# Optimization experiments

Measured on AMD Instinct MI355X. Metric: run time of the kernel, lower is better.

## Reference

```python
import jax, jax.numpy as jnp
import numpy as np

DIM, HEADS, MLP_HID = 1024, 16, 4096
B, N = 2, 2048
EPS = 1e-5

def setup_inputs() -> dict:
    key = jax.random.key(0)
    ks = jax.random.split(key, 8)
    s = lambda fan_in: 1.0 / np.sqrt(fan_in)
    return {
        "x": jax.random.normal(ks[0], (B, N, DIM), jnp.float32),
        "ln1_w": jnp.ones((DIM,), jnp.float32),
        "ln1_b": jnp.zeros((DIM,), jnp.float32),
        # weights stored [in, out] (transpose of torch Linear.weight)
        "qkv_w": jax.random.normal(ks[1], (DIM, 3 * DIM), jnp.float32) * s(DIM),
        "proj_w": jax.random.normal(ks[2], (DIM, DIM), jnp.float32) * s(DIM),
        "proj_b": jnp.zeros((DIM,), jnp.float32),
        "ln2_w": jnp.ones((DIM,), jnp.float32),
        "ln2_b": jnp.zeros((DIM,), jnp.float32),
        "fc1_w": jax.random.normal(ks[3], (DIM, MLP_HID), jnp.float32) * s(DIM),
        "fc1_b": jnp.zeros((MLP_HID,), jnp.float32),
        "fc2_w": jax.random.normal(ks[4], (MLP_HID, DIM), jnp.float32) * s(MLP_HID),
        "fc2_b": jnp.zeros((DIM,), jnp.float32),
    }

def _layernorm(x, w, b):
    mu = jnp.mean(x, axis=-1, keepdims=True)
    var = jnp.mean(jnp.square(x - mu), axis=-1, keepdims=True)
    return (x - mu) * jax.lax.rsqrt(var + EPS) * w + b

def reference(x, ln1_w, ln1_b, qkv_w, proj_w, proj_b, ln2_w, ln2_b, fc1_w, fc1_b, fc2_w, fc2_b):
    Bn, Nn, C = x.shape
    H, D = HEADS, C // HEADS
    scale = D ** -0.5

    # --- attention sub-block (pre-norm, residual) ---
    h = _layernorm(x, ln1_w, ln1_b)
    qkv = (h @ qkv_w).reshape(Bn, Nn, 3, H, D)
    q, k, v = jnp.moveaxis(qkv, 2, 0)  # each [B, N, H, D]
    attn = jnp.einsum('bnhd,bmhd->bhnm', q, k) * scale
    attn = jax.nn.softmax(attn, axis=-1)
    o = jnp.einsum('bhnm,bmhd->bnhd', attn, v).reshape(Bn, Nn, C)
    x = x + (o @ proj_w + proj_b)

    # --- MLP sub-block (pre-norm, residual) ---
    h = _layernorm(x, ln2_w, ln2_b)
    h = jax.nn.gelu(h @ fc1_w + fc1_b, approximate=False)
    x = x + (h @ fc2_w + fc2_b)
    return x
```

## Files before the change

### kernel.cpp

```cpp
#include <hip/hip_runtime.h>
#include <hip/hip_bf16.h>

typedef __attribute__((ext_vector_type(4))) float  f32x4;
typedef __attribute__((ext_vector_type(8))) short  short8;
typedef __attribute__((ext_vector_type(8))) unsigned short ushort8;
typedef __attribute__((ext_vector_type(4))) unsigned short u16x4;
typedef unsigned short u16;

__device__ __forceinline__ u16 f2bf(float f) {
    unsigned int u = __builtin_bit_cast(unsigned int, f);
    return (u16)((u + 0x7fffu + ((u >> 16) & 1u)) >> 16);
}

__device__ __forceinline__ unsigned cvtpk(float lo, float hi) {
    unsigned r;
    asm("v_cvt_pk_bf16_f32 %0, %1, %2" : "=v"(r) : "v"(lo), "v"(hi));
    return r;
}

__device__ __forceinline__ f32x4 mfma16(short8 a, short8 b, f32x4 c) {
    return __builtin_amdgcn_mfma_f32_16x16x32_bf16(a, b, c, 0, 0, 0);
}

__device__ __forceinline__ float fexp2(float x) {
    float r;
    asm("v_exp_f32 %0, %1" : "=v"(r) : "v"(x));
    return r;
}

__device__ __forceinline__ float fgelu(float v) {
    const float t = v * v;
    const float u = v * (-2.302118f - 0.102944f * t);
    return v / (1.0f + fexp2(u));
}

__device__ __forceinline__ void gload_lds16(const u16* g, u16* l) {
    __builtin_amdgcn_global_load_lds(
        (__attribute__((address_space(1))) void*)(uintptr_t)(g),
        (__attribute__((address_space(3))) void*)(unsigned)(uintptr_t)(l),
        16, 0, 0);
}

__device__ __forceinline__ void tcast_body(const float* __restrict__ W,
                                           u16* __restrict__ Wt,
                                           int K, int N, int bx, int by) {
    __shared__ float tile[32][33];
    const int tx = threadIdx.x & 31, ty = threadIdx.x >> 5;
    const int c0 = bx * 32;
    const int r0 = by * 32;
#pragma unroll
    for (int i = 0; i < 32; i += 8)
        tile[ty + i][tx] = W[(size_t)(r0 + ty + i) * N + c0 + tx];
    __syncthreads();
#pragma unroll
    for (int i = 0; i < 32; i += 8)
        Wt[(size_t)(c0 + ty + i) * K + r0 + tx] = f2bf(tile[tx][ty + i]);
}

__device__ __forceinline__ void ln_body(const float* __restrict__ x,
                                        const float* __restrict__ w,
                                        const float* __restrict__ b,
                                        u16* __restrict__ out, int row) {
    const int tid = threadIdx.x;
    const float4 v = ((const float4*)(x + (size_t)row * 1024))[tid];
    float s1 = v.x + v.y + v.z + v.w;
    float s2 = v.x * v.x + v.y * v.y + v.z * v.z + v.w * v.w;
#pragma unroll
    for (int m = 1; m < 64; m <<= 1) { s1 += __shfl_xor(s1, m); s2 += __shfl_xor(s2, m); }
    __shared__ float red1[4], red2[4];
    const int wave = tid >> 6, lane = tid & 63;
    if (lane == 0) { red1[wave] = s1; red2[wave] = s2; }
    __syncthreads();
    s1 = red1[0] + red1[1] + red1[2] + red1[3];
    s2 = red2[0] + red2[1] + red2[2] + red2[3];
    const float mean = s1 * (1.0f / 1024.0f);
    const float var  = s2 * (1.0f / 1024.0f) - mean * mean;
    const float rstd = rsqrtf(var + 1e-5f);
    const float4 wv = ((const float4*)w)[tid];
    const float4 bv = ((const float4*)b)[tid];
    u16x4 o;
    o[0] = f2bf((v.x - mean) * rstd * wv.x + bv.x);
    o[1] = f2bf((v.y - mean) * rstd * wv.y + bv.y);
    o[2] = f2bf((v.z - mean) * rstd * wv.z + bv.z);
    o[3] = f2bf((v.w - mean) * rstd * wv.w + bv.w);
    *(u16x4*)(out + (size_t)row * 1024 + tid * 4) = o;
}

__global__ __launch_bounds__(256) void prep1_kernel(const float* __restrict__ x,
                                                    const float* __restrict__ ln1w,
                                                    const float* __restrict__ ln1b,
                                                    u16* __restrict__ h1,
                                                    const float* __restrict__ qkvw,
                                                    u16* __restrict__ wt_qkv) {
    int id = blockIdx.x;
    if (id < 4096) { ln_body(x, ln1w, ln1b, h1, id); return; }
    id -= 4096;
    tcast_body(qkvw, wt_qkv, 1024, 3072, id % 96, id / 96);
}

__global__ __launch_bounds__(256) void ln_kernel(const float* __restrict__ x,
                                                 const float* __restrict__ w,
                                                 const float* __restrict__ b,
                                                 u16* __restrict__ out) {
    ln_body(x, w, b, out, blockIdx.x);
}

__device__ __forceinline__ void tcast_body512(const float* __restrict__ W,
                                              u16* __restrict__ Wt,
                                              int K, int N, int bx, int by,
                                              float (*tile)[33]) {
    const int tx = threadIdx.x & 31, ty = threadIdx.x >> 5;
    const int c0 = bx * 32;
    const int r0 = by * 32;
#pragma unroll
    for (int i = 0; i < 32; i += 16)
        tile[ty + i][tx] = W[(size_t)(r0 + ty + i) * N + c0 + tx];
    __syncthreads();
#pragma unroll
    for (int i = 0; i < 32; i += 16)
        Wt[(size_t)(c0 + ty + i) * K + r0 + tx] = f2bf(tile[tx][ty + i]);
}

__global__ __launch_bounds__(512, 2) void qkvfused_kernel(const u16* __restrict__ A,
                                                          const u16* __restrict__ Bt,
                                                          u16* __restrict__ Cout,
                                                          u16* __restrict__ vt,
                                                          const float* __restrict__ projw,
                                                          u16* __restrict__ wt_proj,
                                                          const float* __restrict__ fc1w,
                                                          u16* __restrict__ wt_fc1,
                                                          const float* __restrict__ fc2w,
                                                          u16* __restrict__ wt_fc2) {
    __shared__ __align__(16) u16 Ag[3][256 * 32];
    __shared__ __align__(16) u16 Bg[3][128 * 32];
    __shared__ float tile[32][33];
    constexpr int K = 1024, N = 3072;

    if (blockIdx.x >= 384) {
        int id = blockIdx.x - 384;
        if (id < 1024) { tcast_body512(projw, wt_proj, 1024, 1024, id % 32, id / 32, tile); return; }
        id -= 1024;
        if (id < 4096) { tcast_body512(fc1w, wt_fc1, 1024, 4096, id % 128, id / 128, tile); return; }
        id -= 4096;
        tcast_body512(fc2w, wt_fc2, 4096, 1024, id % 32, id / 32, tile);
        return;
    }

    const int tid = threadIdx.x;
    const int wave = tid >> 6, lane = tid & 63;
    const int wr = wave >> 2, wc = wave & 3;
    const int fq = lane >> 4, fr = lane & 15;

    int bid = blockIdx.x;
    bid = (bid & 7) * 48 + (bid >> 3);
    const size_t bm = (size_t)(bid / 24) * 256, bn = (size_t)(bid % 24) * 128;

    const int ko = (fq ^ ((fr >> 1) & 3)) * 8;

    const int srow = tid >> 2;
    const int scol = ((tid & 3) ^ ((tid >> 3) & 3)) * 8;
    const u16* Asrc = A  + (bm + srow) * (size_t)K + scol;
    const u16* Bsrc = Bt + (bn + srow) * (size_t)K + scol;
    const int sdst = wave * 512;

    f32x4 acc[8][2] = {};

    auto STAGE_G = [&](int slot, int kc) {
        gload_lds16(Asrc + kc,                      &Ag[slot][sdst]);
        gload_lds16(Asrc + (size_t)128 * K + kc,    &Ag[slot][sdst + 4096]);
        gload_lds16(Bsrc + kc,                      &Bg[slot][sdst]);
    };

    const int NG = K >> 5;
    STAGE_G(0, 0); STAGE_G(1, 32);
    asm volatile("s_waitcnt vmcnt(3)" ::: "memory");
    __builtin_amdgcn_s_barrier();

    int slot = 0;
    for (int g = 0; g < NG; g++) {
        short8 bfr[2], af[4];
#pragma unroll
        for (int nt = 0; nt < 2; nt++)
            bfr[nt] = *(const short8*)&Bg[slot][(wc * 32 + nt * 16 + fr) * 32 + ko];
#pragma unroll
        for (int m2 = 0; m2 < 4; m2++)
            af[m2] = *(const short8*)&Ag[slot][(wr * 128 + m2 * 16 + fr) * 32 + ko];
        if (g + 2 < NG) {
            const int s2 = slot >= 1 ? slot - 1 : slot + 2;
            STAGE_G(s2, (g + 2) * 32);
        }
        __builtin_amdgcn_s_barrier();
        __builtin_amdgcn_s_setprio(1);
#pragma unroll
        for (int m2 = 0; m2 < 4; m2++)
#pragma unroll
            for (int nt = 0; nt < 2; nt++)
                acc[m2][nt] = mfma16(af[m2], bfr[nt], acc[m2][nt]);
        __builtin_amdgcn_s_setprio(0);
        __builtin_amdgcn_s_barrier();
#pragma unroll
        for (int m2 = 0; m2 < 4; m2++)
            af[m2] = *(const short8*)&Ag[slot][(wr * 128 + (m2 + 4) * 16 + fr) * 32 + ko];
        __builtin_amdgcn_s_barrier();
        __builtin_amdgcn_s_setprio(1);
#pragma unroll
        for (int m2 = 0; m2 < 4; m2++)
#pragma unroll
            for (int nt = 0; nt < 2; nt++)
                acc[m2 + 4][nt] = mfma16(af[m2], bfr[nt], acc[m2 + 4][nt]);
        __builtin_amdgcn_s_setprio(0);
        if (g < NG - 2) { asm volatile("s_waitcnt vmcnt(3)" ::: "memory"); }
        else            { asm volatile("s_waitcnt vmcnt(0)" ::: "memory"); }
        __builtin_amdgcn_s_barrier();
        slot = slot == 2 ? 0 : slot + 1;
    }
    if (bn >= 2048) {
#pragma unroll
        for (int mt = 0; mt < 8; mt++) {
#pragma unroll
            for (int nt = 0; nt < 2; nt++) {
                const size_t col = (bn - 2048) + wc * 32 + nt * 16 + fr;
                const size_t row = bm + wr * 128 + mt * 16 + fq * 4;
                const size_t n = row & 2047, bb = row >> 11;
                u16x4 pw;
#pragma unroll
                for (int j = 0; j < 4; j++) pw[j] = f2bf(acc[mt][nt][j]);
                *(u16x4*)&vt[(bb * 1024 + col) * 2048 + n] = pw;
            }
        }
    } else {
#pragma unroll
        for (int mt = 0; mt < 8; mt++) {
#pragma unroll
            for (int nt = 0; nt < 2; nt++) {
                const size_t col = bn + wc * 32 + nt * 16 + fr;
#pragma unroll
                for (int j = 0; j < 4; j++) {
                    const size_t row = bm + wr * 128 + mt * 16 + fq * 4 + j;
                    Cout[row * N + col] = f2bf(acc[mt][nt][j]);
                }
            }
        }
    }
}

template <int HAS_BIAS, int HAS_RES, int DO_GELU, int OUT_BF16>
__global__ __launch_bounds__(512, 2) void gemm8_kernel(const u16* __restrict__ A,
                                                       const u16* __restrict__ Bt,
                                                       const float* __restrict__ bias,
                                                       const float* __restrict__ res,
                                                       void* __restrict__ Cout,
                                                       int M, int N, int K) {
    __shared__ __align__(16) u16 Ag[3][256 * 32];
    __shared__ __align__(16) u16 Bg[3][128 * 32];
    const int tid = threadIdx.x;
    const int wave = tid >> 6, lane = tid & 63;
    const int wr = wave >> 2, wc = wave & 3;
    const int fq = lane >> 4, fr = lane & 15;

    const int gx = gridDim.x;
    const int nwg = gx * gridDim.y;
    int bid = blockIdx.y * gx + blockIdx.x;
    bid = (bid & 7) * (nwg >> 3) + (bid >> 3);
    const size_t bm = (size_t)(bid / gx) * 256, bn = (size_t)(bid % gx) * 128;

    const int ko = (fq ^ ((fr >> 1) & 3)) * 8;

    const int srow = tid >> 2;
    const int scol = ((tid & 3) ^ ((tid >> 3) & 3)) * 8;
    const u16* Asrc = A  + (bm + srow) * (size_t)K + scol;
    const u16* Bsrc = Bt + (bn + srow) * (size_t)K + scol;
    const int sdst = wave * 512;

    f32x4 acc[8][2] = {};

    auto STAGE_G = [&](int slot, int kc) {
        gload_lds16(Asrc + kc,                      &Ag[slot][sdst]);
        gload_lds16(Asrc + (size_t)128 * K + kc,    &Ag[slot][sdst + 4096]);
        gload_lds16(Bsrc + kc,                      &Bg[slot][sdst]);
    };

    const int NG = K >> 5;
    STAGE_G(0, 0); STAGE_G(1, 32);
    asm volatile("s_waitcnt vmcnt(3)" ::: "memory");
    __builtin_amdgcn_s_barrier();

    int slot = 0;
    for (int g = 0; g < NG; g++) {
        short8 bfr[2], af[4];
#pragma unroll
        for (int nt = 0; nt < 2; nt++)
            bfr[nt] = *(const short8*)&Bg[slot][(wc * 32 + nt * 16 + fr) * 32 + ko];
#pragma unroll
        for (int m2 = 0; m2 < 4; m2++)
            af[m2] = *(const short8*)&Ag[slot][(wr * 128 + m2 * 16 + fr) * 32 + ko];
        if (g + 2 < NG) {
            const int s2 = slot >= 1 ? slot - 1 : slot + 2;
            STAGE_G(s2, (g + 2) * 32);
        }
        __builtin_amdgcn_s_barrier();
        __builtin_amdgcn_s_setprio(1);
#pragma unroll
        for (int m2 = 0; m2 < 4; m2++)
#pragma unroll
            for (int nt = 0; nt < 2; nt++)
                acc[m2][nt] = mfma16(af[m2], bfr[nt], acc[m2][nt]);
        __builtin_amdgcn_s_setprio(0);
        __builtin_amdgcn_s_barrier();
#pragma unroll
        for (int m2 = 0; m2 < 4; m2++)
            af[m2] = *(const short8*)&Ag[slot][(wr * 128 + (m2 + 4) * 16 + fr) * 32 + ko];
        __builtin_amdgcn_s_barrier();
        __builtin_amdgcn_s_setprio(1);
#pragma unroll
        for (int m2 = 0; m2 < 4; m2++)
#pragma unroll
            for (int nt = 0; nt < 2; nt++)
                acc[m2 + 4][nt] = mfma16(af[m2], bfr[nt], acc[m2 + 4][nt]);
        __builtin_amdgcn_s_setprio(0);
        if (g < NG - 2) { asm volatile("s_waitcnt vmcnt(3)" ::: "memory"); }
        else            { asm volatile("s_waitcnt vmcnt(0)" ::: "memory"); }
        __builtin_amdgcn_s_barrier();
        slot = slot == 2 ? 0 : slot + 1;
    }
#pragma unroll
    for (int mt = 0; mt < 8; mt++) {
#pragma unroll
        for (int nt = 0; nt < 2; nt++) {
            const size_t col = bn + wc * 32 + nt * 16 + fr;
            const float bb = HAS_BIAS ? bias[col] : 0.0f;
#pragma unroll
            for (int j = 0; j < 4; j++) {
                const size_t row = bm + wr * 128 + mt * 16 + fq * 4 + j;
                float v = acc[mt][nt][j] + bb;
                if (DO_GELU) v = fgelu(v);
                if (HAS_RES) v += res[row * N + col];
                if (OUT_BF16) ((u16*)Cout)[row * N + col] = f2bf(v);
                else          ((float*)Cout)[row * N + col] = v;
            }
        }
    }
}

template <int HAS_BIAS, int HAS_RES, int DO_GELU, int OUT_BF16>
__global__ __launch_bounds__(256) void gemm64_kernel(const u16* __restrict__ A,
                                                     const u16* __restrict__ Bt,
                                                     const float* __restrict__ bias,
                                                     const float* __restrict__ res,
                                                     void* __restrict__ Cout,
                                                     int M, int N, int K) {
    __shared__ __align__(16) u16 As[2][64 * 64];
    __shared__ __align__(16) u16 Bs[2][128 * 64];
    const int tid = threadIdx.x;
    const int wave = tid >> 6, lane = tid & 63;
    const int wc = wave;
    const int fq = lane >> 4, fr = lane & 15;

    const int gx = gridDim.x;
    const int nwg = gx * gridDim.y;
    int bid = blockIdx.y * gx + blockIdx.x;
    bid = (bid & 7) * (nwg >> 3) + (bid >> 3);
    const size_t bm = (size_t)(bid / gx) * 64, bn = (size_t)(bid % gx) * 128;

    const int lr = lane >> 3, seg = lane & 7;
    const int seg2 = seg ^ lr;

    const u16* Ab = A  + bm * (size_t)K + seg2 * 8;
    const u16* Bb = Bt + bn * (size_t)K + seg2 * 8;

    const int rx = fr & 7;
    const int ko0 = ((0 + fq) ^ rx) * 8;
    const int ko1 = ((4 + fq) ^ rx) * 8;

    f32x4 acc[4][2] = {};

    auto STAGE = [&](int buf, int k0) {
#pragma unroll
        for (int s = 0; s < 2; s++)
            gload_lds16(Ab + (size_t)(s * 32 + wave * 8 + lr) * K + k0,
                        &As[buf][s * 2048 + wave * 512]);
#pragma unroll
        for (int s = 0; s < 4; s++)
            gload_lds16(Bb + (size_t)(s * 32 + wave * 8 + lr) * K + k0,
                        &Bs[buf][s * 2048 + wave * 512]);
    };

    STAGE(0, 0);
    __syncthreads();
    int cur = 0;

    for (int k0 = 0; k0 < K; k0 += 64) {
        if (k0 + 64 < K) STAGE(cur ^ 1, k0 + 64);
#pragma unroll
        for (int ks = 0; ks < 2; ks++) {
            const int ko = ks ? ko1 : ko0;
            short8 af[4], bf[2];
#pragma unroll
            for (int t = 0; t < 4; t++)
                af[t] = *(const short8*)&As[cur][(t * 16 + fr) * 64 + ko];
#pragma unroll
            for (int nt = 0; nt < 2; nt++)
                bf[nt] = *(const short8*)&Bs[cur][(wc * 32 + nt * 16 + fr) * 64 + ko];
#pragma unroll
            for (int mt = 0; mt < 4; mt++)
#pragma unroll
                for (int nt = 0; nt < 2; nt++)
                    acc[mt][nt] = mfma16(af[mt], bf[nt], acc[mt][nt]);
        }
        __syncthreads();
        cur ^= 1;
    }
#pragma unroll
    for (int mt = 0; mt < 4; mt++) {
#pragma unroll
        for (int nt = 0; nt < 2; nt++) {
            const size_t col = bn + wc * 32 + nt * 16 + fr;
            const float bb = HAS_BIAS ? bias[col] : 0.0f;
#pragma unroll
            for (int j = 0; j < 4; j++) {
                const size_t row = bm + mt * 16 + fq * 4 + j;
                float v = acc[mt][nt][j] + bb;
                if (DO_GELU) v = fgelu(v);
                if (HAS_RES) v += res[row * N + col];
                if (OUT_BF16) ((u16*)Cout)[row * N + col] = f2bf(v);
                else          ((float*)Cout)[row * N + col] = v;
            }
        }
    }
}

__global__ __launch_bounds__(512) void attn_kernel(const u16* __restrict__ qkv,
                                                   const u16* __restrict__ vt,
                                                   u16* __restrict__ O) {
    const int bh = blockIdx.x;
    const int b = bh >> 4, h = bh & 15;
    const int qb = blockIdx.y;
    const int tid = threadIdx.x, wave = tid >> 6, lane = tid & 63;
    const int fq = lane >> 4, fr = lane & 15;
    __shared__ __align__(16) u16 Ks[2][64 * 64];
    __shared__ __align__(16) u16 Vs[2][64 * 64];
    __shared__ __align__(16) u16 Pl[8][16 * 64];

    const size_t base = (size_t)b * 2048 * 3072;
    const int q0 = qb * 128 + wave * 16;

    short8 qf[2];
#pragma unroll
    for (int ks = 0; ks < 2; ks++)
        qf[ks] = *(const short8*)(qkv + base + (size_t)(q0 + fr) * 3072 + h * 64 + ks * 32 + fq * 8);

    const int srow = tid >> 3, schunk = tid & 7;
    const int spos = (schunk ^ (srow & 7)) * 8;
    const u16* kdma = qkv + base + 1024 + (size_t)h * 64 + (size_t)srow * 3072 + spos;
    const u16* vdma = vt + ((size_t)b * 1024 + h * 64 + srow) * 2048 + spos;
    const int sdst = wave * 512;

    const int rx = fr & 7;
    const int ko0 = ((0 + fq) ^ rx) * 8;
    const int ko1 = ((4 + fq) ^ rx) * 8;

    f32x4 accO[4] = {};
    float lq = 0.0f;

    const float c = 0.125f * 1.44269504f;

    auto STAGE = [&](int buf, int kt) {
        gload_lds16(kdma + (size_t)kt * 64 * 3072, &Ks[buf][sdst]);
        gload_lds16(vdma + kt * 64,                &Vs[buf][sdst]);
    };

    STAGE(0, 0);
    __syncthreads();
    int cur = 0;

    for (int kt = 0; kt < 32; kt++) {
        if (kt < 31) STAGE(cur ^ 1, kt + 1);
        f32x4 s[4];
#pragma unroll
        for (int nt = 0; nt < 4; nt++) {
            f32x4 a = {};
            short8 kf0 = *(const short8*)&Ks[cur][(nt * 16 + fr) * 64 + ko0];
            short8 kf1 = *(const short8*)&Ks[cur][(nt * 16 + fr) * 64 + ko1];
            a = mfma16(kf0, qf[0], a);
            a = mfma16(kf1, qf[1], a);
            s[nt] = a;
        }
#pragma unroll
        for (int nt = 0; nt < 4; nt++)
#pragma unroll
            for (int j = 0; j < 4; j++) {
                const float pij = fexp2(s[nt][j] * c);
                s[nt][j] = pij;
                lq += pij;
            }
#pragma unroll
        for (int nt = 0; nt < 4; nt++) {
            uint2 pw;
            pw.x = cvtpk(s[nt][0], s[nt][1]);
            pw.y = cvtpk(s[nt][2], s[nt][3]);
            const int chunk = nt * 2 + (fq >> 1);
            *(uint2*)&Pl[wave][fr * 64 + (chunk ^ rx) * 8 + (fq & 1) * 4] = pw;
        }
#pragma unroll
        for (int ks = 0; ks < 2; ks++) {
            const int ko = ks ? ko1 : ko0;
            short8 pf = *(const short8*)&Pl[wave][fr * 64 + ko];
#pragma unroll
            for (int dt = 0; dt < 4; dt++) {
                short8 vf = *(const short8*)&Vs[cur][(dt * 16 + fr) * 64 + ko];
                accO[dt] = mfma16(pf, vf, accO[dt]);
            }
        }
        __syncthreads();
        cur ^= 1;
    }
    lq += __shfl_xor(lq, 16);
    lq += __shfl_xor(lq, 32);
    float rq[4];
#pragma unroll
    for (int j = 0; j < 4; j++) rq[j] = 1.0f / __shfl(lq, fq * 4 + j);
#pragma unroll
    for (int dt = 0; dt < 4; dt++)
#pragma unroll
        for (int j = 0; j < 4; j++) {
            const float v = accO[dt][j] * rq[j];
            O[(size_t)(b * 2048 + q0 + fq * 4 + j) * 1024 + h * 64 + dt * 16 + fr] = f2bf(v);
        }
}

extern "C" void kernel_launch(void* const* d_in, const int* in_sizes, int n_in,
                              void* d_out, int out_size, void* d_ws, size_t ws_size,
                              hipStream_t stream) {
    (void)in_sizes; (void)n_in; (void)out_size; (void)ws_size;
    const float* x     = (const float*)d_in[0];
    const float* ln1w  = (const float*)d_in[1];
    const float* ln1b  = (const float*)d_in[2];
    const float* qkvw  = (const float*)d_in[3];
    const float* projw = (const float*)d_in[4];
    const float* projb = (const float*)d_in[5];
    const float* ln2w  = (const float*)d_in[6];
    const float* ln2b  = (const float*)d_in[7];
    const float* fc1w  = (const float*)d_in[8];
    const float* fc1b  = (const float*)d_in[9];
    const float* fc2w  = (const float*)d_in[10];
    const float* fc2b  = (const float*)d_in[11];

    char* p = (char*)d_ws;
    auto alloc = [&](size_t bytes) { void* r = p; p += (bytes + 255) & ~(size_t)255; return r; };
    u16* wt_qkv  = (u16*)alloc(3072ull * 1024 * 2);
    u16* wt_proj = (u16*)alloc(1024ull * 1024 * 2);
    u16* wt_fc1  = (u16*)alloc(4096ull * 1024 * 2);
    u16* wt_fc2  = (u16*)alloc(1024ull * 4096 * 2);
    u16* h1      = (u16*)alloc(4096ull * 1024 * 2);
    u16* qkv     = (u16*)alloc(4096ull * 3072 * 2);
    u16* vt      = (u16*)alloc(2048ull * 2048 * 2);
    u16* attn_o  = (u16*)alloc(4096ull * 1024 * 2);
    u16* h2      = (u16*)alloc(4096ull * 1024 * 2);
    u16* mlp_h   = (u16*)alloc(4096ull * 4096 * 2);
    float* x1 = (float*)d_out;

    prep1_kernel<<<7168, 256, 0, stream>>>(x, ln1w, ln1b, h1, qkvw, wt_qkv);

    qkvfused_kernel<<<9600, 512, 0, stream>>>(h1, wt_qkv, qkv, vt,
                                              projw, wt_proj, fc1w, wt_fc1, fc2w, wt_fc2);

    attn_kernel<<<dim3(32, 16), 512, 0, stream>>>(qkv, vt, attn_o);
    gemm64_kernel<1, 1, 0, 0><<<dim3(8, 64), 256, 0, stream>>>(attn_o, wt_proj, projb, x, x1, 4096, 1024, 1024);

    ln_kernel<<<4096, 256, 0, stream>>>(x1, ln2w, ln2b, h2);
    gemm8_kernel<1, 0, 1, 1><<<dim3(32, 16), 512, 0, stream>>>(h2, wt_fc1, fc1b, nullptr, mlp_h, 4096, 4096, 1024);
    gemm64_kernel<1, 1, 0, 0><<<dim3(8, 64), 256, 0, stream>>>(mlp_h, wt_fc2, fc2b, x1, d_out, 4096, 1024, 4096);
}
```

Baseline: 222.0 us.

## Fold softmax scale into Q epilogue, compute row sums via MFMA, stage V transpose in LDS

The QKV GEMM epilogue now multiplies Q columns by the softmax scale times log2(e), so the attention loop applies exp2 directly without a per-element multiply. Softmax row sums are computed by an extra MFMA of the bf16 P fragment against a ones vector, replacing the scalar accumulation and cross-lane shuffles. The V-transpose writes are first staged through LDS, reusing the GEMM buffers, and then written out as coalesced 16-byte rows. The trade-offs are that the row sums now come from bf16-rounded probabilities, Q is rounded after scaling, and the epilogue gains an extra block barrier.

```diff
diff --git a/kernel.cpp b/kernel.cpp
--- a/kernel.cpp
+++ b/kernel.cpp
@@ -131,9 +131,10 @@
                                                           u16* __restrict__ wt_fc1,
                                                           const float* __restrict__ fc2w,
                                                           u16* __restrict__ wt_fc2) {
-    __shared__ __align__(16) u16 Ag[3][256 * 32];
-    __shared__ __align__(16) u16 Bg[3][128 * 32];
-    __shared__ float tile[32][33];
+    __shared__ __align__(16) u16 smem[38976];
+    u16* Agp = smem;
+    u16* Bgp = smem + 24576;
+    float (*tile)[33] = (float(*)[33])(smem + 36864);
     constexpr int K = 1024, N = 3072;
 
     if (blockIdx.x >= 384) {
@@ -166,9 +167,9 @@
     f32x4 acc[8][2] = {};
 
     auto STAGE_G = [&](int slot, int kc) {
-        gload_lds16(Asrc + kc,                      &Ag[slot][sdst]);
-        gload_lds16(Asrc + (size_t)128 * K + kc,    &Ag[slot][sdst + 4096]);
-        gload_lds16(Bsrc + kc,                      &Bg[slot][sdst]);
+        gload_lds16(Asrc + kc,                      Agp + slot * 8192 + sdst);
+        gload_lds16(Asrc + (size_t)128 * K + kc,    Agp + slot * 8192 + sdst + 4096);
+        gload_lds16(Bsrc + kc,                      Bgp + slot * 4096 + sdst);
     };
 
     const int NG = K >> 5;
@@ -181,10 +182,10 @@
         short8 bfr[2], af[4];
 #pragma unroll
         for (int nt = 0; nt < 2; nt++)
-            bfr[nt] = *(const short8*)&Bg[slot][(wc * 32 + nt * 16 + fr) * 32 + ko];
-#pragma unroll
-        for (int m2 = 0; m2 < 4; m2++)
-            af[m2] = *(const short8*)&Ag[slot][(wr * 128 + m2 * 16 + fr) * 32 + ko];
+            bfr[nt] = *(const short8*)&Bgp[slot * 4096 + (wc * 32 + nt * 16 + fr) * 32 + ko];
+#pragma unroll
+        for (int m2 = 0; m2 < 4; m2++)
+            af[m2] = *(const short8*)&Agp[slot * 8192 + (wr * 128 + m2 * 16 + fr) * 32 + ko];
         if (g + 2 < NG) {
             const int s2 = slot >= 1 ? slot - 1 : slot + 2;
             STAGE_G(s2, (g + 2) * 32);
@@ -200,7 +201,7 @@
         __builtin_amdgcn_s_barrier();
 #pragma unroll
         for (int m2 = 0; m2 < 4; m2++)
-            af[m2] = *(const short8*)&Ag[slot][(wr * 128 + (m2 + 4) * 16 + fr) * 32 + ko];
+            af[m2] = *(const short8*)&Agp[slot * 8192 + (wr * 128 + (m2 + 4) * 16 + fr) * 32 + ko];
         __builtin_amdgcn_s_barrier();
         __builtin_amdgcn_s_setprio(1);
 #pragma unroll
@@ -214,21 +215,35 @@
         __builtin_amdgcn_s_barrier();
         slot = slot == 2 ? 0 : slot + 1;
     }
+
     if (bn >= 2048) {
+        constexpr int VP = 264;
+        u16* vbuf = smem;
 #pragma unroll
         for (int mt = 0; mt < 8; mt++) {
 #pragma unroll
             for (int nt = 0; nt < 2; nt++) {
-                const size_t col = (bn - 2048) + wc * 32 + nt * 16 + fr;
-                const size_t row = bm + wr * 128 + mt * 16 + fq * 4;
-                const size_t n = row & 2047, bb = row >> 11;
+                const int col = wc * 32 + nt * 16 + fr;
+                const int tok = wr * 128 + mt * 16 + fq * 4;
                 u16x4 pw;
 #pragma unroll
                 for (int j = 0; j < 4; j++) pw[j] = f2bf(acc[mt][nt][j]);
-                *(u16x4*)&vt[(bb * 1024 + col) * 2048 + n] = pw;
+                *(u16x4*)&vbuf[col * VP + tok] = pw;
             }
         }
+        __syncthreads();
+        const size_t vc0 = bn - 2048;
+        const size_t bb = bm >> 11;
+        const size_t tk0 = bm & 2047;
+#pragma unroll
+        for (int i = 0; i < 8; i++) {
+            const int idx = i * 512 + tid;
+            const int col = idx >> 5, ch = idx & 31;
+            ushort8 v = *(const ushort8*)&vbuf[col * VP + ch * 8];
+            *(ushort8*)&vt[(bb * 1024 + vc0 + col) * 2048 + tk0 + ch * 8] = v;
+        }
     } else {
+        const float qscale = (bn < 1024) ? 0.125f * 1.44269504f : 1.0f;
 #pragma unroll
         for (int mt = 0; mt < 8; mt++) {
 #pragma unroll
@@ -237,7 +252,7 @@
 #pragma unroll
                 for (int j = 0; j < 4; j++) {
                     const size_t row = bm + wr * 128 + mt * 16 + fq * 4 + j;
-                    Cout[row * N + col] = f2bf(acc[mt][nt][j]);
+                    Cout[row * N + col] = f2bf(acc[mt][nt][j] * qscale);
                 }
             }
         }
@@ -460,9 +475,10 @@
     const int ko1 = ((4 + fq) ^ rx) * 8;
 
     f32x4 accO[4] = {};
-    float lq = 0.0f;
-
-    const float c = 0.125f * 1.44269504f;
+    f32x4 accL = {};
+    short8 ones;
+#pragma unroll
+    for (int j = 0; j < 8; j++) ones[j] = (short)0x3F80;
 
     auto STAGE = [&](int buf, int kt) {
         gload_lds16(kdma + (size_t)kt * 64 * 3072, &Ks[buf][sdst]);
@@ -488,11 +504,8 @@
 #pragma unroll
         for (int nt = 0; nt < 4; nt++)
 #pragma unroll
-            for (int j = 0; j < 4; j++) {
-                const float pij = fexp2(s[nt][j] * c);
-                s[nt][j] = pij;
-                lq += pij;
-            }
+            for (int j = 0; j < 4; j++)
+                s[nt][j] = fexp2(s[nt][j]);
 #pragma unroll
         for (int nt = 0; nt < 4; nt++) {
             uint2 pw;
@@ -505,6 +518,7 @@
         for (int ks = 0; ks < 2; ks++) {
             const int ko = ks ? ko1 : ko0;
             short8 pf = *(const short8*)&Pl[wave][fr * 64 + ko];
+            accL = mfma16(pf, ones, accL);
 #pragma unroll
             for (int dt = 0; dt < 4; dt++) {
                 short8 vf = *(const short8*)&Vs[cur][(dt * 16 + fr) * 64 + ko];
@@ -514,11 +528,9 @@
         __syncthreads();
         cur ^= 1;
     }
-    lq += __shfl_xor(lq, 16);
-    lq += __shfl_xor(lq, 32);
     float rq[4];
 #pragma unroll
-    for (int j = 0; j < 4; j++) rq[j] = 1.0f / __shfl(lq, fq * 4 + j);
+    for (int j = 0; j < 4; j++) rq[j] = 1.0f / accL[j];
 #pragma unroll
     for (int dt = 0; dt < 4; dt++)
 #pragma unroll
```

Result: faster. 202.8 us, median of 2 (-8.7%).
